# Kernel tuning notes

Hardware: AMD Instinct MI355X
Metric: run time of the kernel (lower is better)

Reference implementation:

```python
import jax, jax.numpy as jnp
import numpy as np

B, L, H, T, C = 64, 1024, 512, 100, 97


def setup_inputs() -> dict:
    key = jax.random.key(0)
    k1, k2, k3, k4, k5 = jax.random.split(key, 5)
    return {
        "position_fmap": jax.random.normal(k1, (B, L, H), dtype=jnp.float32),
        "origin_fmap": jax.random.normal(k2, (B, L, H), dtype=jnp.float32),
        "pos_emb": jax.random.normal(k3, (T, H), dtype=jnp.float32),
        "W_gen": jax.random.normal(k4, (C, H), dtype=jnp.float32) * (1.0 / np.sqrt(H)),
        "b_gen": jax.random.normal(k5, (C,), dtype=jnp.float32) * 0.01,
    }


def reference(position_fmap, origin_fmap, pos_emb, W_gen, b_gen):
    # The torch loop over t in [0, T) computes, per step, scores = fmap @ emb_t,
    # softmax over L, then context = a^T @ origin_fmap. Batched over all steps:
    scores = jnp.einsum('blh,th->btl', position_fmap, pos_emb)   # [B, T, L]
    attn = jax.nn.softmax(scores, axis=-1)                       # softmax over spatial L
    context = jnp.einsum('btl,blh->bth', attn, origin_fmap)      # [B, T, H]
    # generator: Linear(H -> num_classes)
    return jnp.einsum('bth,ch->btc', context, W_gen) + b_gen     # [B, T, C]
```

## Files before the change

kernel.cpp:

```cpp
#include <hip/hip_runtime.h>
#include <hip/hip_bf16.h>

#define B_   64
#define L_   1024
#define H_   512
#define T_   100
#define C_   97
#define TP_  112

typedef _Float16 h8 __attribute__((ext_vector_type(8)));
typedef __attribute__((ext_vector_type(4))) float f32x4;

__global__ __launch_bounds__(256) void k0_prep(
    const float* __restrict__ emb, const float* __restrict__ W,
    _Float16* __restrict__ embh, _Float16* __restrict__ Wh) {
  const int row = blockIdx.x, tid = threadIdx.x;
  if (row < TP_) {
    for (int j = tid; j < H_; j += 256)
      embh[(size_t)row * H_ + j] =
          (row < T_) ? (_Float16)emb[(size_t)row * H_ + j] : (_Float16)0.f;
  } else {
    const int c = row - TP_;
    for (int j = tid; j < H_; j += 256)
      Wh[(size_t)c * H_ + j] =
          (c < C_) ? (_Float16)W[(size_t)c * H_ + j] : (_Float16)0.f;
  }
}

__global__ __launch_bounds__(256) void k1_scores(
    const float* __restrict__ fmap, const _Float16* __restrict__ embh,
    _Float16* __restrict__ sc, float* __restrict__ part) {
  __shared__ float red_m[4 * TP_];
  __shared__ float red_s[4 * TP_];
  __shared__ float sMb[TP_];
  const int tid = threadIdx.x;
  const int wave = tid >> 6, lane = tid & 63;
  const int quad = lane >> 4, cc = lane & 15;
  const int m0 = blockIdx.x * 128 + wave * 32;

  f32x4 acc0[7], acc1[7];
#pragma unroll
  for (int i = 0; i < 7; ++i) {
    acc0[i] = (f32x4){0.f, 0.f, 0.f, 0.f};
    acc1[i] = (f32x4){0.f, 0.f, 0.f, 0.f};
  }

  const float* a0p = fmap + (size_t)(m0 + cc) * H_ + quad * 8;
  const float* a1p = a0p + (size_t)16 * H_;
#pragma unroll 2
  for (int k = 0; k < H_; k += 32) {
    float4 x0 = *(const float4*)(a0p + k);
    float4 x1 = *(const float4*)(a0p + k + 4);
    float4 y0 = *(const float4*)(a1p + k);
    float4 y1 = *(const float4*)(a1p + k + 4);
    h8 a0, a1;
    a0[0] = (_Float16)x0.x; a0[1] = (_Float16)x0.y;
    a0[2] = (_Float16)x0.z; a0[3] = (_Float16)x0.w;
    a0[4] = (_Float16)x1.x; a0[5] = (_Float16)x1.y;
    a0[6] = (_Float16)x1.z; a0[7] = (_Float16)x1.w;
    a1[0] = (_Float16)y0.x; a1[1] = (_Float16)y0.y;
    a1[2] = (_Float16)y0.z; a1[3] = (_Float16)y0.w;
    a1[4] = (_Float16)y1.x; a1[5] = (_Float16)y1.y;
    a1[6] = (_Float16)y1.z; a1[7] = (_Float16)y1.w;
#pragma unroll
    for (int i = 0; i < 7; ++i) {
      h8 bf = *(const h8*)(embh + (size_t)(i * 16 + cc) * H_ + k + quad * 8);
      acc0[i] = __builtin_amdgcn_mfma_f32_16x16x32_f16(a0, bf, acc0[i], 0, 0, 0);
      acc1[i] = __builtin_amdgcn_mfma_f32_16x16x32_f16(a1, bf, acc1[i], 0, 0, 0);
    }
  }

  float pm[7], ps[7];
#pragma unroll
  for (int i = 0; i < 7; ++i) {
    float m = acc0[i][0];
#pragma unroll
    for (int r = 1; r < 4; ++r) m = fmaxf(m, acc0[i][r]);
#pragma unroll
    for (int r = 0; r < 4; ++r) m = fmaxf(m, acc1[i][r]);
    float s = 0.f;
#pragma unroll
    for (int r = 0; r < 4; ++r) s += __expf(acc0[i][r] - m) + __expf(acc1[i][r] - m);
    pm[i] = m; ps[i] = s;
  }
#pragma unroll
  for (int d = 16; d < 64; d <<= 1) {
#pragma unroll
    for (int i = 0; i < 7; ++i) {
      float om = __shfl_xor(pm[i], d, 64);
      float os = __shfl_xor(ps[i], d, 64);
      float M = fmaxf(pm[i], om);
      ps[i] = ps[i] * __expf(pm[i] - M) + os * __expf(om - M);
      pm[i] = M;
    }
  }
  if (lane < 16) {
#pragma unroll
    for (int i = 0; i < 7; ++i) {
      red_m[wave * TP_ + i * 16 + lane] = pm[i];
      red_s[wave * TP_ + i * 16 + lane] = ps[i];
    }
  }
  __syncthreads();
  if (tid < TP_) {
    float M = red_m[tid], S = red_s[tid];
#pragma unroll
    for (int w = 1; w < 4; ++w) {
      float om = red_m[w * TP_ + tid], os = red_s[w * TP_ + tid];
      float nM = fmaxf(M, om);
      S = S * __expf(M - nM) + os * __expf(om - nM);
      M = nM;
    }
    float* p = part + ((size_t)blockIdx.x * TP_ + tid) * 2;
    p[0] = M; p[1] = S;
    sMb[tid] = M;
  }
  __syncthreads();
#pragma unroll
  for (int i = 0; i < 7; ++i) {
    float mb = sMb[i * 16 + cc];
#pragma unroll
    for (int r = 0; r < 4; ++r) {
      const int row0 = m0 + quad * 4 + r;
      sc[(size_t)row0 * TP_ + i * 16 + cc]        = (_Float16)(acc0[i][r] - mb);
      sc[(size_t)(row0 + 16) * TP_ + i * 16 + cc] = (_Float16)(acc1[i][r] - mb);
    }
  }
}

__global__ __launch_bounds__(256) void k2_softmax(
    const _Float16* __restrict__ sc, const float* __restrict__ part,
    _Float16* __restrict__ attn) {
  __shared__ float sAdj[TP_], sInv[TP_];
  const int b = blockIdx.x >> 3, lblk = blockIdx.x & 7;
  const int tid = threadIdx.x;
  if (tid < TP_) {
    float M = -1e30f, S = 0.f;
    for (int k = 0; k < 8; ++k) {
      const float* p = part + ((size_t)(b * 8 + k) * TP_ + tid) * 2;
      float om = p[0], os = p[1];
      float nM = fmaxf(M, om);
      S = S * __expf(M - nM) + os * __expf(om - nM);
      M = nM;
    }
    sInv[tid] = 1.f / S;
    sAdj[tid] = part[((size_t)(b * 8 + lblk) * TP_ + tid) * 2] - M;
  }
  __syncthreads();
  const _Float16* sp = sc + (size_t)blockIdx.x * (128 * TP_);
  _Float16* ap = attn + (size_t)blockIdx.x * (128 * TP_);
  for (int f = tid * 8; f < 128 * TP_; f += 2048) {
    h8 v = *(const h8*)(sp + f);
    const int t0 = f % TP_;
    h8 o;
#pragma unroll
    for (int j = 0; j < 8; ++j)
      o[j] = (_Float16)(__expf((float)v[j] + sAdj[t0 + j]) * sInv[t0 + j]);
    *(h8*)(ap + f) = o;
  }
}

__global__ __launch_bounds__(256) void k3_context(
    const _Float16* __restrict__ attn, const float* __restrict__ origin,
    float* __restrict__ ctxT) {
  const int b = blockIdx.x >> 3, hb = (blockIdx.x & 7) * 64;
  const int tid = threadIdx.x;
  const int wave = tid >> 6, lane = tid & 63;
  const int quad = lane >> 4, cc = lane & 15;
  const int hA = hb + wave * 16 + cc;

  f32x4 acc[7];
#pragma unroll
  for (int i = 0; i < 7; ++i) acc[i] = (f32x4){0.f, 0.f, 0.f, 0.f};

  const float* op = origin + (size_t)b * L_ * H_ + (size_t)(quad * 8) * H_ + hA;
  const _Float16* bp = attn + (size_t)b * L_ * TP_ + (size_t)(quad * 8) * TP_;

#pragma unroll 2
  for (int l0 = 0; l0 < L_; l0 += 32) {
    h8 a;
#pragma unroll
    for (int j = 0; j < 8; ++j) a[j] = (_Float16)op[(size_t)(l0 + j) * H_];
#pragma unroll
    for (int i = 0; i < 7; ++i) {
      h8 bf;
#pragma unroll
      for (int j = 0; j < 8; ++j) bf[j] = bp[(size_t)(l0 + j) * TP_ + i * 16 + cc];
      acc[i] = __builtin_amdgcn_mfma_f32_16x16x32_f16(a, bf, acc[i], 0, 0, 0);
    }
  }
  const int hrow = hb + wave * 16 + quad * 4;
#pragma unroll
  for (int i = 0; i < 7; ++i)
#pragma unroll
    for (int r = 0; r < 4; ++r)
      ctxT[((size_t)b * H_ + hrow + r) * TP_ + i * 16 + cc] = acc[i][r];
}

__global__ __launch_bounds__(256) void k4_out(
    const float* __restrict__ ctxT, const _Float16* __restrict__ Wh,
    const float* __restrict__ bias, float* __restrict__ out) {
  const int b = blockIdx.x / 7, mt = blockIdx.x % 7;
  const int tid = threadIdx.x;
  const int wave = tid >> 6, lane = tid & 63;
  const int quad = lane >> 4, cc = lane & 15;
  f32x4 acc0 = (f32x4){0.f, 0.f, 0.f, 0.f};
  f32x4 acc1 = (f32x4){0.f, 0.f, 0.f, 0.f};
  const int c0 = wave * 16 + cc;
  const int c1 = (wave + 4) * 16 + cc;
  const bool hasB = (wave < 3);
  const float* apc = ctxT + ((size_t)b * H_ + quad * 8) * TP_ + mt * 16 + cc;
  const _Float16* b0p = Wh + (size_t)c0 * H_ + quad * 8;
  const _Float16* b1p = Wh + (size_t)(hasB ? c1 : c0) * H_ + quad * 8;
  for (int k = 0; k < H_; k += 32) {
    h8 a;
#pragma unroll
    for (int j = 0; j < 8; ++j) a[j] = (_Float16)apc[(size_t)(k + j) * TP_];
    h8 bf0 = *(const h8*)(b0p + k);
    acc0 = __builtin_amdgcn_mfma_f32_16x16x32_f16(a, bf0, acc0, 0, 0, 0);
    if (hasB) {
      h8 bf1 = *(const h8*)(b1p + k);
      acc1 = __builtin_amdgcn_mfma_f32_16x16x32_f16(a, bf1, acc1, 0, 0, 0);
    }
  }
  const float bias0 = (c0 < C_) ? bias[c0] : 0.f;
  const float bias1 = (hasB && c1 < C_) ? bias[c1] : 0.f;
#pragma unroll
  for (int r = 0; r < 4; ++r) {
    const int t = mt * 16 + quad * 4 + r;
    if (t < T_) {
      if (c0 < C_) out[((size_t)b * T_ + t) * C_ + c0] = acc0[r] + bias0;
      if (hasB && c1 < C_) out[((size_t)b * T_ + t) * C_ + c1] = acc1[r] + bias1;
    }
  }
}

extern "C" void kernel_launch(void* const* d_in, const int* in_sizes, int n_in,
                              void* d_out, int out_size, void* d_ws, size_t ws_size,
                              hipStream_t stream) {
  const float* fmap   = (const float*)d_in[0];
  const float* origin = (const float*)d_in[1];
  const float* emb    = (const float*)d_in[2];
  const float* W      = (const float*)d_in[3];
  const float* bias   = (const float*)d_in[4];
  float* out = (float*)d_out;

  char* ws = (char*)d_ws;
  _Float16* embh = (_Float16*)(ws);
  _Float16* Wh   = (_Float16*)(ws + 114688);
  _Float16* sc   = (_Float16*)(ws + 229376);
  float*    part = (float*)   (ws + 14909440);
  _Float16* attn = (_Float16*)(ws + 15368192);
  float*    ctxT = (float*)   (ws + 30048256);

  hipLaunchKernelGGL(k0_prep,    dim3(224), dim3(256), 0, stream, emb, W, embh, Wh);
  hipLaunchKernelGGL(k1_scores,  dim3(512), dim3(256), 0, stream, fmap, embh, sc, part);
  hipLaunchKernelGGL(k2_softmax, dim3(512), dim3(256), 0, stream, sc, part, attn);
  hipLaunchKernelGGL(k3_context, dim3(512), dim3(256), 0, stream, attn, origin, ctxT);
  hipLaunchKernelGGL(k4_out,     dim3(448), dim3(256), 0, stream, ctxT, Wh, bias, out);
}
```

Baseline: 364.4 us.

## Transpose scores/attention to T-major layout and store context in fp16

Scores are staged through shared memory and written T-major (t, l), so the context GEMM can load attention operands as contiguous 8-wide fp16 vectors instead of strided scalar gathers. k1 now uses 64-row blocks with one accumulator set per wave and twice as many blocks, and the softmax kernel is reorganised to handle 14 rows of t per block with 16 partial maxima per batch. Context is written as fp16 [B,T,H], so the output GEMM reads it with vector loads instead of strided fp32 loads. The cost is extra shared-memory traffic and a barrier in k1, plus another fp16 rounding of the context.

```diff
diff --git a/kernel.cpp b/kernel.cpp
--- a/kernel.cpp
+++ b/kernel.cpp
@@ -27,60 +27,49 @@
   }
 }
 
-__global__ __launch_bounds__(256) void k1_scores(
+__global__ __launch_bounds__(256, 4) void k1_scores(
     const float* __restrict__ fmap, const _Float16* __restrict__ embh,
-    _Float16* __restrict__ sc, float* __restrict__ part) {
+    _Float16* __restrict__ scT, float* __restrict__ part) {
   __shared__ float red_m[4 * TP_];
   __shared__ float red_s[4 * TP_];
   __shared__ float sMb[TP_];
+  __shared__ _Float16 tile[TP_ * 72];
   const int tid = threadIdx.x;
   const int wave = tid >> 6, lane = tid & 63;
   const int quad = lane >> 4, cc = lane & 15;
-  const int m0 = blockIdx.x * 128 + wave * 32;
-
-  f32x4 acc0[7], acc1[7];
-#pragma unroll
-  for (int i = 0; i < 7; ++i) {
-    acc0[i] = (f32x4){0.f, 0.f, 0.f, 0.f};
-    acc1[i] = (f32x4){0.f, 0.f, 0.f, 0.f};
-  }
-
-  const float* a0p = fmap + (size_t)(m0 + cc) * H_ + quad * 8;
-  const float* a1p = a0p + (size_t)16 * H_;
+  const int b = blockIdx.x >> 4;
+  const int m0 = blockIdx.x * 64 + wave * 16;
+
+  f32x4 acc[7];
+#pragma unroll
+  for (int i = 0; i < 7; ++i) acc[i] = (f32x4){0.f, 0.f, 0.f, 0.f};
+
+  const float* ap = fmap + (size_t)(m0 + cc) * H_ + quad * 8;
 #pragma unroll 2
   for (int k = 0; k < H_; k += 32) {
-    float4 x0 = *(const float4*)(a0p + k);
-    float4 x1 = *(const float4*)(a0p + k + 4);
-    float4 y0 = *(const float4*)(a1p + k);
-    float4 y1 = *(const float4*)(a1p + k + 4);
-    h8 a0, a1;
-    a0[0] = (_Float16)x0.x; a0[1] = (_Float16)x0.y;
-    a0[2] = (_Float16)x0.z; a0[3] = (_Float16)x0.w;
-    a0[4] = (_Float16)x1.x; a0[5] = (_Float16)x1.y;
-    a0[6] = (_Float16)x1.z; a0[7] = (_Float16)x1.w;
-    a1[0] = (_Float16)y0.x; a1[1] = (_Float16)y0.y;
-    a1[2] = (_Float16)y0.z; a1[3] = (_Float16)y0.w;
-    a1[4] = (_Float16)y1.x; a1[5] = (_Float16)y1.y;
-    a1[6] = (_Float16)y1.z; a1[7] = (_Float16)y1.w;
+    float4 x0 = *(const float4*)(ap + k);
+    float4 x1 = *(const float4*)(ap + k + 4);
+    h8 a;
+    a[0] = (_Float16)x0.x; a[1] = (_Float16)x0.y;
+    a[2] = (_Float16)x0.z; a[3] = (_Float16)x0.w;
+    a[4] = (_Float16)x1.x; a[5] = (_Float16)x1.y;
+    a[6] = (_Float16)x1.z; a[7] = (_Float16)x1.w;
 #pragma unroll
     for (int i = 0; i < 7; ++i) {
       h8 bf = *(const h8*)(embh + (size_t)(i * 16 + cc) * H_ + k + quad * 8);
-      acc0[i] = __builtin_amdgcn_mfma_f32_16x16x32_f16(a0, bf, acc0[i], 0, 0, 0);
-      acc1[i] = __builtin_amdgcn_mfma_f32_16x16x32_f16(a1, bf, acc1[i], 0, 0, 0);
+      acc[i] = __builtin_amdgcn_mfma_f32_16x16x32_f16(a, bf, acc[i], 0, 0, 0);
     }
   }
 
   float pm[7], ps[7];
 #pragma unroll
   for (int i = 0; i < 7; ++i) {
-    float m = acc0[i][0];
-#pragma unroll
-    for (int r = 1; r < 4; ++r) m = fmaxf(m, acc0[i][r]);
-#pragma unroll
-    for (int r = 0; r < 4; ++r) m = fmaxf(m, acc1[i][r]);
+    float m = acc[i][0];
+#pragma unroll
+    for (int r = 1; r < 4; ++r) m = fmaxf(m, acc[i][r]);
     float s = 0.f;
 #pragma unroll
-    for (int r = 0; r < 4; ++r) s += __expf(acc0[i][r] - m) + __expf(acc1[i][r] - m);
+    for (int r = 0; r < 4; ++r) s += __expf(acc[i][r] - m);
     pm[i] = m; ps[i] = s;
   }
 #pragma unroll
@@ -120,85 +109,91 @@
   for (int i = 0; i < 7; ++i) {
     float mb = sMb[i * 16 + cc];
 #pragma unroll
-    for (int r = 0; r < 4; ++r) {
-      const int row0 = m0 + quad * 4 + r;
-      sc[(size_t)row0 * TP_ + i * 16 + cc]        = (_Float16)(acc0[i][r] - mb);
-      sc[(size_t)(row0 + 16) * TP_ + i * 16 + cc] = (_Float16)(acc1[i][r] - mb);
-    }
+    for (int r = 0; r < 4; ++r)
+      tile[(i * 16 + cc) * 72 + wave * 16 + quad * 4 + r] = (_Float16)(acc[i][r] - mb);
+  }
+  __syncthreads();
+  _Float16* dst = scT + (size_t)b * TP_ * L_ + (size_t)(blockIdx.x & 15) * 64;
+  for (int idx = tid; idx < 896; idx += 256) {
+    const int t = idx >> 3, c = idx & 7;
+    h8 v = *(const h8*)&tile[t * 72 + c * 8];
+    *(h8*)(dst + (size_t)t * L_ + c * 8) = v;
   }
 }
 
 __global__ __launch_bounds__(256) void k2_softmax(
-    const _Float16* __restrict__ sc, const float* __restrict__ part,
-    _Float16* __restrict__ attn) {
-  __shared__ float sAdj[TP_], sInv[TP_];
-  const int b = blockIdx.x >> 3, lblk = blockIdx.x & 7;
-  const int tid = threadIdx.x;
-  if (tid < TP_) {
+    const _Float16* __restrict__ scT, const float* __restrict__ part,
+    _Float16* __restrict__ attnT) {
+  __shared__ float sAdj[16 * 14];
+  __shared__ float sInv[14];
+  const int b = blockIdx.x >> 3, tg = blockIdx.x & 7;
+  const int tid = threadIdx.x;
+  if (tid < 14) {
+    const int t = tg * 14 + tid;
     float M = -1e30f, S = 0.f;
-    for (int k = 0; k < 8; ++k) {
-      const float* p = part + ((size_t)(b * 8 + k) * TP_ + tid) * 2;
+    for (int k = 0; k < 16; ++k) {
+      const float* p = part + ((size_t)(b * 16 + k) * TP_ + t) * 2;
       float om = p[0], os = p[1];
       float nM = fmaxf(M, om);
       S = S * __expf(M - nM) + os * __expf(om - nM);
       M = nM;
     }
     sInv[tid] = 1.f / S;
-    sAdj[tid] = part[((size_t)(b * 8 + lblk) * TP_ + tid) * 2] - M;
-  }
-  __syncthreads();
-  const _Float16* sp = sc + (size_t)blockIdx.x * (128 * TP_);
-  _Float16* ap = attn + (size_t)blockIdx.x * (128 * TP_);
-  for (int f = tid * 8; f < 128 * TP_; f += 2048) {
-    h8 v = *(const h8*)(sp + f);
-    const int t0 = f % TP_;
+    for (int k = 0; k < 16; ++k)
+      sAdj[k * 14 + tid] = part[((size_t)(b * 16 + k) * TP_ + t) * 2] - M;
+  }
+  __syncthreads();
+  const size_t base = ((size_t)b * TP_ + tg * 14) * L_;
+  for (int idx = tid; idx < 14 * 128; idx += 256) {
+    const int t = idx >> 7, c = idx & 127;
+    const size_t off = base + (size_t)t * L_ + c * 8;
+    h8 v = *(const h8*)(scT + off);
+    const float adj = sAdj[(c >> 3) * 14 + t];
+    const float inv = sInv[t];
     h8 o;
 #pragma unroll
     for (int j = 0; j < 8; ++j)
-      o[j] = (_Float16)(__expf((float)v[j] + sAdj[t0 + j]) * sInv[t0 + j]);
-    *(h8*)(ap + f) = o;
+      o[j] = (_Float16)(__expf((float)v[j] + adj) * inv);
+    *(h8*)(attnT + off) = o;
   }
 }
 
 __global__ __launch_bounds__(256) void k3_context(
-    const _Float16* __restrict__ attn, const float* __restrict__ origin,
-    float* __restrict__ ctxT) {
+    const _Float16* __restrict__ attnT, const float* __restrict__ origin,
+    _Float16* __restrict__ ctx) {
   const int b = blockIdx.x >> 3, hb = (blockIdx.x & 7) * 64;
   const int tid = threadIdx.x;
   const int wave = tid >> 6, lane = tid & 63;
   const int quad = lane >> 4, cc = lane & 15;
-  const int hA = hb + wave * 16 + cc;
 
   f32x4 acc[7];
 #pragma unroll
   for (int i = 0; i < 7; ++i) acc[i] = (f32x4){0.f, 0.f, 0.f, 0.f};
 
-  const float* op = origin + (size_t)b * L_ * H_ + (size_t)(quad * 8) * H_ + hA;
-  const _Float16* bp = attn + (size_t)b * L_ * TP_ + (size_t)(quad * 8) * TP_;
+  const _Float16* aA = attnT + ((size_t)b * TP_ + cc) * L_ + quad * 8;
+  const float* bp = origin + ((size_t)b * L_ + quad * 8) * H_ + hb + wave * 16 + cc;
 
 #pragma unroll 2
   for (int l0 = 0; l0 < L_; l0 += 32) {
-    h8 a;
-#pragma unroll
-    for (int j = 0; j < 8; ++j) a[j] = (_Float16)op[(size_t)(l0 + j) * H_];
-#pragma unroll
-    for (int i = 0; i < 7; ++i) {
-      h8 bf;
-#pragma unroll
-      for (int j = 0; j < 8; ++j) bf[j] = bp[(size_t)(l0 + j) * TP_ + i * 16 + cc];
-      acc[i] = __builtin_amdgcn_mfma_f32_16x16x32_f16(a, bf, acc[i], 0, 0, 0);
-    }
-  }
-  const int hrow = hb + wave * 16 + quad * 4;
+    h8 bfh;
+#pragma unroll
+    for (int j = 0; j < 8; ++j) bfh[j] = (_Float16)bp[(size_t)(l0 + j) * H_];
+#pragma unroll
+    for (int i = 0; i < 7; ++i) {
+      h8 af = *(const h8*)(aA + (size_t)(i * 16) * L_ + l0);
+      acc[i] = __builtin_amdgcn_mfma_f32_16x16x32_f16(af, bfh, acc[i], 0, 0, 0);
+    }
+  }
+  const int h = hb + wave * 16 + cc;
 #pragma unroll
   for (int i = 0; i < 7; ++i)
 #pragma unroll
     for (int r = 0; r < 4; ++r)
-      ctxT[((size_t)b * H_ + hrow + r) * TP_ + i * 16 + cc] = acc[i][r];
+      ctx[((size_t)b * TP_ + i * 16 + quad * 4 + r) * H_ + h] = (_Float16)acc[i][r];
 }
 
 __global__ __launch_bounds__(256) void k4_out(
-    const float* __restrict__ ctxT, const _Float16* __restrict__ Wh,
+    const _Float16* __restrict__ ctx, const _Float16* __restrict__ Wh,
     const float* __restrict__ bias, float* __restrict__ out) {
   const int b = blockIdx.x / 7, mt = blockIdx.x % 7;
   const int tid = threadIdx.x;
@@ -209,18 +204,17 @@
   const int c0 = wave * 16 + cc;
   const int c1 = (wave + 4) * 16 + cc;
   const bool hasB = (wave < 3);
-  const float* apc = ctxT + ((size_t)b * H_ + quad * 8) * TP_ + mt * 16 + cc;
+  const _Float16* ap  = ctx + ((size_t)b * TP_ + mt * 16 + cc) * H_ + quad * 8;
   const _Float16* b0p = Wh + (size_t)c0 * H_ + quad * 8;
   const _Float16* b1p = Wh + (size_t)(hasB ? c1 : c0) * H_ + quad * 8;
+#pragma unroll 2
   for (int k = 0; k < H_; k += 32) {
-    h8 a;
-#pragma unroll
-    for (int j = 0; j < 8; ++j) a[j] = (_Float16)apc[(size_t)(k + j) * TP_];
+    h8 af = *(const h8*)(ap + k);
     h8 bf0 = *(const h8*)(b0p + k);
-    acc0 = __builtin_amdgcn_mfma_f32_16x16x32_f16(a, bf0, acc0, 0, 0, 0);
+    acc0 = __builtin_amdgcn_mfma_f32_16x16x32_f16(af, bf0, acc0, 0, 0, 0);
     if (hasB) {
       h8 bf1 = *(const h8*)(b1p + k);
-      acc1 = __builtin_amdgcn_mfma_f32_16x16x32_f16(a, bf1, acc1, 0, 0, 0);
+      acc1 = __builtin_amdgcn_mfma_f32_16x16x32_f16(af, bf1, acc1, 0, 0, 0);
     }
   }
   const float bias0 = (c0 < C_) ? bias[c0] : 0.f;
@@ -246,16 +240,16 @@
   float* out = (float*)d_out;
 
   char* ws = (char*)d_ws;
-  _Float16* embh = (_Float16*)(ws);
-  _Float16* Wh   = (_Float16*)(ws + 114688);
-  _Float16* sc   = (_Float16*)(ws + 229376);
-  float*    part = (float*)   (ws + 14909440);
-  _Float16* attn = (_Float16*)(ws + 15368192);
-  float*    ctxT = (float*)   (ws + 30048256);
-
-  hipLaunchKernelGGL(k0_prep,    dim3(224), dim3(256), 0, stream, emb, W, embh, Wh);
-  hipLaunchKernelGGL(k1_scores,  dim3(512), dim3(256), 0, stream, fmap, embh, sc, part);
-  hipLaunchKernelGGL(k2_softmax, dim3(512), dim3(256), 0, stream, sc, part, attn);
-  hipLaunchKernelGGL(k3_context, dim3(512), dim3(256), 0, stream, attn, origin, ctxT);
-  hipLaunchKernelGGL(k4_out,     dim3(448), dim3(256), 0, stream, ctxT, Wh, bias, out);
-}
+  _Float16* embh  = (_Float16*)(ws);
+  _Float16* Wh    = (_Float16*)(ws + 114688);
+  _Float16* scT   = (_Float16*)(ws + 229376);
+  float*    part  = (float*)   (ws + 14909440);
+  _Float16* attnT = (_Float16*)(ws + 15826944);
+  _Float16* ctx   = (_Float16*)(ws + 30507008);
+
+  hipLaunchKernelGGL(k0_prep,    dim3(224),  dim3(256), 0, stream, emb, W, embh, Wh);
+  hipLaunchKernelGGL(k1_scores,  dim3(1024), dim3(256), 0, stream, fmap, embh, scT, part);
+  hipLaunchKernelGGL(k2_softmax, dim3(512),  dim3(256), 0, stream, scT, part, attnT);
+  hipLaunchKernelGGL(k3_context, dim3(512),  dim3(256), 0, stream, attnT, origin, ctx);
+  hipLaunchKernelGGL(k4_out,     dim3(448),  dim3(256), 0, stream, ctx, Wh, bias, out);
+}
```

Result: slower. 375.7 us (+3.1%).
